# Optimization experiments

Measured on AMD Instinct MI355X. Metric: run time of the kernel, lower is better.

## Reference

```python
import jax, jax.numpy as jnp
import numpy as np
from functools import partial

WIDTH = 2560
LRU = 2560
HEADS = 8
DCONV = 4
B = 4
L = 2048


def setup_inputs() -> dict:
    key = jax.random.key(0)
    ks = jax.random.split(key, 16)
    bw = LRU // HEADS
    x = jax.random.normal(ks[0], (B, L, WIDTH), dtype=jnp.float32)
    segment_pos = jnp.broadcast_to(jnp.arange(L, dtype=jnp.int32), (B, L))
    # indices of the last DCONV frames of the left-padded conv input (length L+DCONV-1)
    base = (jnp.arange(DCONV, dtype=jnp.int32) + (L - 1))
    conv_idx = jnp.broadcast_to(base, (B, LRU, DCONV))
    s = 0.02
    return {
        "x": x,
        "segment_pos": segment_pos,
        "conv_idx": conv_idx,
        "Wx": jax.random.normal(ks[1], (LRU, WIDTH), jnp.float32) * s,
        "bx": jax.random.normal(ks[2], (LRU,), jnp.float32) * s,
        "Wy": jax.random.normal(ks[3], (LRU, WIDTH), jnp.float32) * s,
        "conv_w": jax.random.normal(ks[4], (LRU, DCONV), jnp.float32) * s,  # depthwise kernel
        "conv_b": jax.random.normal(ks[5], (LRU,), jnp.float32) * s,
        "gx_w": jax.random.normal(ks[6], (HEADS, bw, bw), jnp.float32) * s,
        "gx_b": jax.random.normal(ks[7], (HEADS, bw), jnp.float32) * s,
        "ga_w": jax.random.normal(ks[8], (HEADS, bw, bw), jnp.float32) * s,
        "ga_b": jax.random.normal(ks[9], (HEADS, bw), jnp.float32) * s,
        "a_param": jax.random.normal(ks[10], (LRU,), jnp.float32),
        "y_bias": jax.random.normal(ks[11], (1, 1, LRU), jnp.float32) * s,
        "Wout": jax.random.normal(ks[12], (WIDTH, LRU), jnp.float32) * s,
        "bout": jax.random.normal(ks[13], (WIDTH,), jnp.float32) * s,
    }


def _block_diag(x, w):
    # x: [B,L,(h*i)], w: [h,i,j] -> [B,L,(h*j)]
    b, l, _ = x.shape
    h, bw, _ = w.shape
    xb = x.reshape(b, l, h, bw)
    y = jnp.einsum('blhi,hij->blhj', xb, w)
    return y.reshape(b, l, h * bw)


def _scan_op(c1, c2):
    a1, b1 = c1
    a2, b2 = c2
    return (a1 * a2, a2 * b1 + b2)


def reference(x, segment_pos, conv_idx, Wx, bx, Wy, conv_w, conv_b,
              gx_w, gx_b, ga_w, ga_b, a_param, y_bias, Wout, bout):
    dc = conv_w.shape[1]
    seqlen = x.shape[1]

    y = jnp.einsum('bld,ed->ble', x, Wy)                 # linear_y (no bias)
    xl = jnp.einsum('bld,ed->ble', x, Wx) + bx           # linear_x

    # causal depthwise conv1d, padding dc-1 on the left, keep first seqlen
    xpad = jnp.pad(xl, ((0, 0), (dc - 1, 0), (0, 0)))    # [B, L+dc-1, LRU]
    xc = conv_b + sum(conv_w[:, k] * xpad[:, k:k + seqlen, :] for k in range(dc))

    # conv_state: gather of padded (channels-first) input at conv_idx
    conv_state = jnp.take_along_axis(xpad.transpose(0, 2, 1), conv_idx.astype(jnp.int32), axis=2)

    gx = _block_diag(xc, gx_w)  # fuse_bias=True: bias added inside rg_lru
    ga = _block_diag(xc, ga_w)

    # rg_lru_ref
    reset = (segment_pos == 0).astype(x.dtype)[..., None]        # [B,L,1]
    gate_x = jax.nn.sigmoid(gx + gx_b.reshape(-1))
    gate_a = jax.nn.sigmoid(ga + ga_b.reshape(-1))
    c = -8.0 * jax.nn.softplus(a_param)
    log_a = c * gate_a
    a = jnp.exp(log_a) * (1.0 - reset)
    multiplier = jnp.sqrt(1.0 - jnp.exp(2.0 * log_a))
    multiplier = reset + (1.0 - reset) * multiplier
    normalized_x = xc * gate_x * multiplier

    _, h = jax.lax.associative_scan(_scan_op, (a, normalized_x), axis=1)
    last_h = h[:, -1]

    out = h * jax.nn.gelu(y + y_bias, approximate=False)
    out = jnp.einsum('ble,de->bld', out, Wout) + bout    # linear_out
    return out, conv_state, last_h
```

## Files before the change

kernel.cpp:

```cpp
#include <hip/hip_runtime.h>
#include <hip/hip_bf16.h>

#define WIDTH_ 2560
#define LRU_   2560
#define HEADS_ 8
#define BW_    320
#define DCONV_ 4
#define BB     4
#define LL     2048
#define MROWS  (BB*LL)
#define NCH    32
#define CLEN   (LL/NCH)

typedef unsigned short ushort_t;
typedef __attribute__((ext_vector_type(8))) short short8;
typedef __attribute__((ext_vector_type(4))) float f32x4;

__device__ __forceinline__ unsigned short f2bf(float f) {
  union { float f; unsigned u; } v; v.f = f;
  unsigned r = v.u + 0x7fffu + ((v.u >> 16) & 1u);
  return (unsigned short)(r >> 16);
}
__device__ __forceinline__ float bf2f(unsigned short h) {
  union { unsigned u; float f; } v; v.u = ((unsigned)h) << 16;
  return v.f;
}
__device__ __forceinline__ void async_load16(const void* g, void* l) {
  __builtin_amdgcn_global_load_lds(
      (const __attribute__((address_space(1))) unsigned*)g,
      (__attribute__((address_space(3))) unsigned*)l, 16, 0, 0);
}
__device__ __forceinline__ float sigmoidf_(float x) {
  return 1.f / (1.f + __expf(-x));
}

__global__ void cvt_bf16x4(const float4* __restrict__ in, ushort4* __restrict__ out, int n4) {
  int i = blockIdx.x * blockDim.x + threadIdx.x;
  if (i >= n4) return;
  float4 v = in[i];
  ushort4 o;
  o.x = f2bf(v.x); o.y = f2bf(v.y); o.z = f2bf(v.z); o.w = f2bf(v.w);
  out[i] = o;
}

__global__ void cvt_transpose(const float* __restrict__ w, ushort_t* __restrict__ gwT,
                              int rowoff, int n) {
  int i = blockIdx.x * blockDim.x + threadIdx.x;
  if (i >= n) return;
  int ii = i % BW_;
  int j  = (i / BW_) % BW_;
  int h  = i / (BW_ * BW_);
  gwT[((size_t)h * 640 + rowoff + j) * BW_ + ii] = f2bf(w[((size_t)h * BW_ + ii) * BW_ + j]);
}

__global__ void ctab_kernel(const float* __restrict__ apar, float* __restrict__ ctab) {
  int e = blockIdx.x * blockDim.x + threadIdx.x;
  if (e >= LRU_) return;
  float ap = apar[e];
  float sp = (ap > 15.f) ? ap : log1pf(expf(ap));
  ctab[e] = -8.f * sp;
}

template<int EPI>
__global__ __launch_bounds__(512, 2)
void gemm8p(const ushort_t* __restrict__ A,
            const ushort_t* __restrict__ B,
            void* __restrict__ C0, void* __restrict__ C1,
            const float* __restrict__ bias) {
  constexpr int LDA = 2560, KK = 2560, NT = KK / 64, MT = 32;
  __shared__ char smem[131072];
  const int tid = threadIdx.x;
  const int lane = tid & 63, w = tid >> 6;
  const int wr = w >> 2, wc = w & 3;
  const int l15 = lane & 15, l4 = lane >> 4;

  const int nblk = gridDim.x;
  const int bid = blockIdx.x;
  const int swz = (bid & 7) * (nblk >> 3) + (bid >> 3);
  const int tm = (swz % MT) * 256;
  const int tn = (swz / MT) * 256;

  unsigned aoff[4], boff[4]; int ldst[4];
#pragma unroll
  for (int h = 0; h < 2; ++h)
#pragma unroll
    for (int j = 0; j < 2; ++j) {
      int lb = (j * 512 + tid) * 16;
      int lbl = lb ^ (((lb >> 9) & 1) << 5);
      int row = lbl >> 7, colb = lbl & 127;
      aoff[h * 2 + j] = (unsigned)(tm + h * 128 + row) * (LDA * 2) + colb;
      boff[h * 2 + j] = (unsigned)(tn + h * 128 + row) * (KK * 2) + colb;
      ldst[h * 2 + j] = h * 16384 + lb;
    }

  auto STAGE_A = [&](int kt, int p) {
#pragma unroll
    for (int u = 0; u < 4; ++u)
      async_load16((const char*)A + (size_t)aoff[u] + (unsigned)kt * 128,
                   smem + p * 32768 + ldst[u]);
  };
  auto STAGE_B = [&](int kt, int p) {
#pragma unroll
    for (int u = 0; u < 4; ++u)
      async_load16((const char*)B + (size_t)boff[u] + (unsigned)kt * 128,
                   smem + 65536 + p * 32768 + ldst[u]);
  };
  auto LDFRAG = [&](const char* half, int row, int sbyte) -> short8 {
    int lb = row * 128 + sbyte;
    lb ^= ((lb >> 9) & 1) << 5;
    return *(const short8*)(half + lb);
  };

  f32x4 acc[8][4] = {};

  STAGE_A(0, 0); STAGE_B(0, 0);
  asm volatile("s_waitcnt vmcnt(0)" ::: "memory");
  __builtin_amdgcn_s_barrier();

  for (int t = 0; t < NT; ++t) {
    const int p = t & 1;
    const char* Ah = smem + p * 32768 + wr * 16384;
    const char* Bh = smem + 65536 + p * 32768 + (wc >> 1) * 16384;
    const int bcol0 = (wc & 1) * 64;
    short8 bfrag[4][2];
    const bool st = (t + 1 < NT);
#pragma unroll
    for (int q = 0; q < 4; ++q) {
      short8 a[2][2];
#pragma unroll
      for (int mm = 0; mm < 2; ++mm)
#pragma unroll
        for (int s = 0; s < 2; ++s)
          a[mm][s] = LDFRAG(Ah, (2 * q + mm) * 16 + l15, s * 64 + l4 * 16);
      if (q == 0) {
#pragma unroll
        for (int n = 0; n < 4; ++n)
#pragma unroll
          for (int s = 0; s < 2; ++s)
            bfrag[n][s] = LDFRAG(Bh, bcol0 + n * 16 + l15, s * 64 + l4 * 16);
        if (st) STAGE_A(t + 1, p ^ 1);
      }
      if (q == 1 && st) STAGE_B(t + 1, p ^ 1);
      __builtin_amdgcn_s_barrier();
      __builtin_amdgcn_s_setprio(1);
#pragma unroll
      for (int mm = 0; mm < 2; ++mm)
#pragma unroll
        for (int n = 0; n < 4; ++n)
#pragma unroll
          for (int s = 0; s < 2; ++s)
            acc[2 * q + mm][n] = __builtin_amdgcn_mfma_f32_16x16x32_bf16(
                a[mm][s], bfrag[n][s], acc[2 * q + mm][n], 0, 0, 0);
      __builtin_amdgcn_s_setprio(0);
      if (q == 3) asm volatile("s_waitcnt vmcnt(0)" ::: "memory");
      __builtin_amdgcn_s_barrier();
    }
  }

  const int crow0 = tm + wr * 128 + l4 * 4;
  const int ccol0 = tn + wc * 64 + l15;
#pragma unroll
  for (int m = 0; m < 8; ++m)
#pragma unroll
    for (int n = 0; n < 4; ++n) {
      const int col = ccol0 + n * 16;
#pragma unroll
      for (int r = 0; r < 4; ++r) {
        const int row = crow0 + m * 16 + r;
        float v = acc[m][n][r];
        if (EPI == 0) {
          ((float*)C0)[(size_t)row * 2560 + col] = v + bias[col];
        } else {
          if (col < 2560)
            ((ushort_t*)C0)[(size_t)row * 2560 + col] = f2bf(v + bias[col]);
          else
            ((ushort_t*)C1)[(size_t)row * 2560 + (col - 2560)] = f2bf(v);
        }
      }
    }
}

__global__ __launch_bounds__(256, 2)
void gate_gemm(const ushort_t* __restrict__ A,
               const ushort_t* __restrict__ Bw,
               ushort_t* __restrict__ GX,
               ushort_t* __restrict__ AAo,
               const float* __restrict__ gxb, const float* __restrict__ gab,
               const float* __restrict__ ctab, const int* __restrict__ seg) {
  constexpr int BM = 128, BN = 64, BK = 32, WTN = 32, NF = 2;
  __shared__ ushort_t lds_a[BM * BK];
  __shared__ ushort_t lds_b[BN * BK];

  const int tid = threadIdx.x;
  const int w = tid >> 6, lane = tid & 63;
  const int wr = w >> 1, wc = w & 1;
  const int tm = blockIdx.x * BM;
  const int tn = blockIdx.y * BN;
  const int z = blockIdx.z;
  const ushort_t* Ab = A + (size_t)z * BW_;
  const ushort_t* Bb = Bw + (size_t)z * 640 * BW_ + (size_t)tn * BW_;

  f32x4 acc[4][NF] = {};
  const int ksub = (lane >> 4) * 8;
  const int rA = wr * 64 + (lane & 15);
  const int rB = wc * WTN + (lane & 15);

  for (int k0 = 0; k0 < BW_; k0 += BK) {
#pragma unroll
    for (int i = 0; i < 2; ++i) {
      int bo = (i * 256 + tid) * 16;
      int row = bo >> 6, colb = bo & 63;
      async_load16((const char*)Ab + (size_t)(tm + row) * LRU_ * 2 + (size_t)k0 * 2 + colb,
                   (char*)lds_a + bo);
    }
    {
      int bo = tid * 16;
      int row = bo >> 6, colb = bo & 63;
      async_load16((const char*)Bb + (size_t)row * BW_ * 2 + (size_t)k0 * 2 + colb,
                   (char*)lds_b + bo);
    }
    __syncthreads();
    short8 af[4], bfr[NF];
#pragma unroll
    for (int mf = 0; mf < 4; ++mf)
      af[mf] = *(const short8*)&lds_a[(rA + mf * 16) * BK + ksub];
#pragma unroll
    for (int nf = 0; nf < NF; ++nf)
      bfr[nf] = *(const short8*)&lds_b[(rB + nf * 16) * BK + ksub];
#pragma unroll
    for (int mf = 0; mf < 4; ++mf)
#pragma unroll
      for (int nf = 0; nf < NF; ++nf)
        acc[mf][nf] = __builtin_amdgcn_mfma_f32_16x16x32_bf16(af[mf], bfr[nf], acc[mf][nf], 0, 0, 0);
    __syncthreads();
  }

  const int crow0 = tm + wr * 64 + ((lane >> 4) << 2);
  const int ccol0 = tn + wc * WTN + (lane & 15);
#pragma unroll
  for (int mf = 0; mf < 4; ++mf) {
#pragma unroll
    for (int nf = 0; nf < NF; ++nf) {
      const int cih = ccol0 + nf * 16;
#pragma unroll
      for (int r = 0; r < 4; ++r) {
        const int row = crow0 + mf * 16 + r;
        if (cih < BW_) {
          const int gc = z * BW_ + cih;
          float v = acc[mf][nf][r] + gxb[gc];
          float xc = bf2f(A[(size_t)row * LRU_ + gc]);
          GX[(size_t)row * LRU_ + gc] = f2bf(xc * sigmoidf_(v));
        } else {
          const int gc = z * BW_ + cih - BW_;
          float v = acc[mf][nf][r] + gab[gc];
          float la = ctab[gc] * sigmoidf_(v);
          float av = (seg[row] == 0) ? 0.f : expf(la);
          AAo[(size_t)row * LRU_ + gc] = f2bf(av);
        }
      }
    }
  }
}

__global__ void conv_kernel(const ushort_t* __restrict__ xl, const float* __restrict__ convw,
                            const float* __restrict__ convb, ushort_t* __restrict__ xcbf) {
  int i = blockIdx.x * blockDim.x + threadIdx.x;
  if (i >= MROWS * LRU_ / 8) return;
  int e0 = (i % (LRU_ / 8)) * 8;
  int t = (i / (LRU_ / 8)) % LL;
  int b = i / ((LRU_ / 8) * LL);
  size_t rowb = ((size_t)b * LL + t) * LRU_;
  const ushort_t* base = xl + rowb + e0;
  short8 v0 = {}, v1 = {}, v2 = {}, v3;
  if (t >= 3) v0 = *(const short8*)(base - 3 * LRU_);
  if (t >= 2) v1 = *(const short8*)(base - 2 * LRU_);
  if (t >= 1) v2 = *(const short8*)(base - 1 * LRU_);
  v3 = *(const short8*)(base);
  ushort_t o[8];
#pragma unroll
  for (int u = 0; u < 8; ++u) {
    float4 wv = ((const float4*)convw)[e0 + u];
    float acc = convb[e0 + u];
    acc += wv.x * bf2f((ushort_t)v0[u]);
    acc += wv.y * bf2f((ushort_t)v1[u]);
    acc += wv.z * bf2f((ushort_t)v2[u]);
    acc += wv.w * bf2f((ushort_t)v3[u]);
    o[u] = f2bf(acc);
  }
  *(short8*)(xcbf + rowb + e0) = *(short8*)o;
}

__global__ void conv_state_kernel(const ushort_t* __restrict__ xl, const int* __restrict__ cidx,
                                  float* __restrict__ cs) {
  int i = blockIdx.x * blockDim.x + threadIdx.x;
  if (i >= BB * LRU_ * DCONV_) return;
  int e = (i / DCONV_) % LRU_;
  int b = i / (DCONV_ * LRU_);
  int idx = cidx[i];
  int ts = idx - (DCONV_ - 1);
  float v = 0.f;
  if (ts >= 0 && ts < LL) v = bf2f(xl[((size_t)b * LL + ts) * LRU_ + e]);
  cs[i] = v;
}

__global__ void scanA(const ushort_t* __restrict__ AA, const ushort_t* __restrict__ GX,
                      float* __restrict__ cA, float* __restrict__ cH) {
  int i = blockIdx.x * blockDim.x + threadIdx.x;
  if (i >= BB * NCH * LRU_) return;
  int e = i % LRU_;
  int c = (i / LRU_) % NCH;
  int b = i / (LRU_ * NCH);
  float Ap = 1.f, h = 0.f;
  size_t base = ((size_t)b * LL + (size_t)c * CLEN) * LRU_ + e;
  for (int t = 0; t < CLEN; ++t) {
    size_t j = base + (size_t)t * LRU_;
    float a = bf2f(AA[j]);
    float nx = bf2f(GX[j]) * sqrtf(fmaxf(0.f, 1.f - a * a));
    Ap *= a;
    h = a * h + nx;
  }
  cA[i] = Ap; cH[i] = h;
}

__global__ void scanB(const float* __restrict__ cA, const float* __restrict__ cH,
                      float* __restrict__ hInit) {
  int i = blockIdx.x * blockDim.x + threadIdx.x;
  if (i >= BB * LRU_) return;
  int e = i % LRU_;
  int b = i / LRU_;
  float h = 0.f;
  for (int c = 0; c < NCH; ++c) {
    size_t j = ((size_t)b * NCH + c) * LRU_ + e;
    hInit[j] = h;
    h = cA[j] * h + cH[j];
  }
}

__global__ void scanC(const ushort_t* __restrict__ AA, const ushort_t* __restrict__ GXpre,
                      const float* __restrict__ hInit, const ushort_t* __restrict__ ybf,
                      const float* __restrict__ ybias, float* __restrict__ lastH) {
  int i = blockIdx.x * blockDim.x + threadIdx.x;
  if (i >= BB * NCH * LRU_) return;
  int e = i % LRU_;
  int c = (i / LRU_) % NCH;
  int b = i / (LRU_ * NCH);
  float h = hInit[i];
  float yb = ybias[e];
  ushort_t* pre = (ushort_t*)GXpre;
  size_t base = ((size_t)b * LL + (size_t)c * CLEN) * LRU_ + e;
  for (int t = 0; t < CLEN; ++t) {
    size_t j = base + (size_t)t * LRU_;
    float a = bf2f(AA[j]);
    float nx = bf2f(GXpre[j]) * sqrtf(fmaxf(0.f, 1.f - a * a));
    h = a * h + nx;
    float yv = bf2f(ybf[j]) + yb;
    float g = 0.5f * yv * (1.f + erff(yv * 0.70710678118f));
    pre[j] = f2bf(h * g);
  }
  if (c == NCH - 1) lastH[(size_t)b * LRU_ + e] = h;
}

extern "C" void kernel_launch(void* const* d_in, const int* in_sizes, int n_in,
                              void* d_out, int out_size, void* d_ws, size_t ws_size,
                              hipStream_t stream) {
  const float* x     = (const float*)d_in[0];
  const int*   seg   = (const int*)d_in[1];
  const int*   cidx  = (const int*)d_in[2];
  const float* Wx    = (const float*)d_in[3];
  const float* bx    = (const float*)d_in[4];
  const float* Wy    = (const float*)d_in[5];
  const float* convw = (const float*)d_in[6];
  const float* convb = (const float*)d_in[7];
  const float* gxw   = (const float*)d_in[8];
  const float* gxb   = (const float*)d_in[9];
  const float* gaw   = (const float*)d_in[10];
  const float* gab   = (const float*)d_in[11];
  const float* apar  = (const float*)d_in[12];
  const float* ybias = (const float*)d_in[13];
  const float* Wout  = (const float*)d_in[14];
  const float* bout  = (const float*)d_in[15];

  float* out    = (float*)d_out;
  float* cs_out = out + (size_t)MROWS * WIDTH_;
  float* lh_out = cs_out + (size_t)BB * LRU_ * DCONV_;

  ushort_t* ybf = (ushort_t*)d_out;
  ushort_t* AA  = (ushort_t*)((char*)d_out + (size_t)41943040);

  const size_t SZ_BIG = (size_t)MROWS * LRU_ * 2;
  const size_t SZ_WC  = (size_t)(2 * LRU_) * WIDTH_ * 2;
  const size_t SZ_GW  = (size_t)HEADS_ * 640 * BW_ * 2;
  const size_t SZ_SM  = (size_t)BB * NCH * LRU_ * 4;
  size_t need = SZ_BIG * 3 + SZ_WC + SZ_GW + 10240 + SZ_SM * 3;
  if (ws_size < need) return;

  char* p = (char*)d_ws;
  ushort_t* xbf   = (ushort_t*)p; p += SZ_BIG;
  ushort_t* wcat  = (ushort_t*)p; p += SZ_WC;
  ushort_t* T2    = (ushort_t*)p; p += SZ_BIG;
  ushort_t* xcbf  = (ushort_t*)p; p += SZ_BIG;
  ushort_t* gwT   = (ushort_t*)p; p += SZ_GW;
  float*    ctab  = (float*)p;    p += 10240;
  float*    cA    = (float*)p;    p += SZ_SM;
  float*    cH    = (float*)p;    p += SZ_SM;
  float*    hInit = (float*)p;    p += SZ_SM;
  ushort_t* woutbf = wcat;

  const int BLK = 256;
  cvt_bf16x4<<<(MROWS * WIDTH_ / 4 + BLK - 1) / BLK, BLK, 0, stream>>>(
      (const float4*)x, (ushort4*)xbf, MROWS * WIDTH_ / 4);
  cvt_bf16x4<<<(LRU_ * WIDTH_ / 4 + BLK - 1) / BLK, BLK, 0, stream>>>(
      (const float4*)Wx, (ushort4*)wcat, LRU_ * WIDTH_ / 4);
  cvt_bf16x4<<<(LRU_ * WIDTH_ / 4 + BLK - 1) / BLK, BLK, 0, stream>>>(
      (const float4*)Wy, (ushort4*)(wcat + (size_t)LRU_ * WIDTH_), LRU_ * WIDTH_ / 4);

  gemm8p<1><<<640, 512, 0, stream>>>(xbf, wcat, T2, ybf, bx);

  cvt_bf16x4<<<(WIDTH_ * LRU_ / 4 + BLK - 1) / BLK, BLK, 0, stream>>>(
      (const float4*)Wout, (ushort4*)woutbf, WIDTH_ * LRU_ / 4);

  conv_kernel<<<(MROWS * LRU_ / 8 + BLK - 1) / BLK, BLK, 0, stream>>>(T2, convw, convb, xcbf);
  conv_state_kernel<<<(BB * LRU_ * DCONV_ + BLK - 1) / BLK, BLK, 0, stream>>>(T2, cidx, cs_out);

  cvt_transpose<<<(HEADS_ * BW_ * BW_ + BLK - 1) / BLK, BLK, 0, stream>>>(gxw, gwT, 0, HEADS_ * BW_ * BW_);
  cvt_transpose<<<(HEADS_ * BW_ * BW_ + BLK - 1) / BLK, BLK, 0, stream>>>(gaw, gwT, BW_, HEADS_ * BW_ * BW_);
  ctab_kernel<<<(LRU_ + BLK - 1) / BLK, BLK, 0, stream>>>(apar, ctab);

  gate_gemm<<<dim3(MROWS / 128, 10, HEADS_), BLK, 0, stream>>>(
      xcbf, gwT, T2, AA, gxb, gab, ctab, seg);

  scanA<<<(BB * NCH * LRU_ + BLK - 1) / BLK, BLK, 0, stream>>>(AA, T2, cA, cH);
  scanB<<<(BB * LRU_ + BLK - 1) / BLK, BLK, 0, stream>>>(cA, cH, hInit);
  scanC<<<(BB * NCH * LRU_ + BLK - 1) / BLK, BLK, 0, stream>>>(AA, T2, hInit, ybf, ybias, lh_out);

  gemm8p<0><<<320, 512, 0, stream>>>(T2, woutbf, out, nullptr, bout);
}
```

Before: 685.9 us.

## Rework bf16 GEMM main loop into 4-stage BK=32 async-copy ring

The GEMM main loop changes from a double-buffered 64-wide K step with 8 barriers per step to a 4-slot ring of 32-wide K slices. Loads run three stages ahead with graded vmcnt waits and a single barrier per step. The shared-memory layout becomes k-chunk-major with no XOR swizzle, so fragment reads are simple strided 16-byte loads. The block-to-tile mapping is also rewritten. The goal is to cut barrier and synchronisation overhead and hide global-load latency better. The cost is smaller K steps and more outstanding memory operations per wavefront.

```diff
diff --git a/kernel.cpp b/kernel.cpp
--- a/kernel.cpp
+++ b/kernel.cpp
@@ -67,7 +67,7 @@
             const ushort_t* __restrict__ B,
             void* __restrict__ C0, void* __restrict__ C1,
             const float* __restrict__ bias) {
-  constexpr int LDA = 2560, KK = 2560, NT = KK / 64, MT = 32;
+  constexpr int KK = 2560, NT = KK / 32;
   __shared__ char smem[131072];
   const int tid = threadIdx.x;
   const int lane = tid & 63, w = tid >> 6;
@@ -75,86 +75,74 @@
   const int l15 = lane & 15, l4 = lane >> 4;
 
   const int nblk = gridDim.x;
-  const int bid = blockIdx.x;
-  const int swz = (bid & 7) * (nblk >> 3) + (bid >> 3);
-  const int tm = (swz % MT) * 256;
-  const int tn = (swz / MT) * 256;
-
-  unsigned aoff[4], boff[4]; int ldst[4];
-#pragma unroll
-  for (int h = 0; h < 2; ++h)
-#pragma unroll
-    for (int j = 0; j < 2; ++j) {
-      int lb = (j * 512 + tid) * 16;
-      int lbl = lb ^ (((lb >> 9) & 1) << 5);
-      int row = lbl >> 7, colb = lbl & 127;
-      aoff[h * 2 + j] = (unsigned)(tm + h * 128 + row) * (LDA * 2) + colb;
-      boff[h * 2 + j] = (unsigned)(tn + h * 128 + row) * (KK * 2) + colb;
-      ldst[h * 2 + j] = h * 16384 + lb;
-    }
-
-  auto STAGE_A = [&](int kt, int p) {
-#pragma unroll
-    for (int u = 0; u < 4; ++u)
-      async_load16((const char*)A + (size_t)aoff[u] + (unsigned)kt * 128,
-                   smem + p * 32768 + ldst[u]);
-  };
-  auto STAGE_B = [&](int kt, int p) {
-#pragma unroll
-    for (int u = 0; u < 4; ++u)
-      async_load16((const char*)B + (size_t)boff[u] + (unsigned)kt * 128,
-                   smem + 65536 + p * 32768 + ldst[u]);
-  };
-  auto LDFRAG = [&](const char* half, int row, int sbyte) -> short8 {
-    int lb = row * 128 + sbyte;
-    lb ^= ((lb >> 9) & 1) << 5;
-    return *(const short8*)(half + lb);
-  };
+  const int TN = nblk >> 5;
+  const int x8 = blockIdx.x & 7, c = blockIdx.x >> 3;
+  const int tm = (x8 * 4 + c / TN) * 256;
+  const int tn = (c % TN) * 256;
+
+  const char* aSrc[2]; const char* bSrc[2]; int ldst[2];
+#pragma unroll
+  for (int u = 0; u < 2; ++u) {
+    int lb = (u * 512 + tid) * 16;
+    int ks = lb >> 12, m = (lb >> 4) & 255;
+    aSrc[u] = (const char*)A + (size_t)(tm + m) * (KK * 2) + ks * 16;
+    bSrc[u] = (const char*)B + (size_t)(tn + m) * (KK * 2) + ks * 16;
+    ldst[u] = lb;
+  }
 
   f32x4 acc[8][4] = {};
 
-  STAGE_A(0, 0); STAGE_B(0, 0);
-  asm volatile("s_waitcnt vmcnt(0)" ::: "memory");
-  __builtin_amdgcn_s_barrier();
+#pragma unroll
+  for (int kt = 0; kt < 3; ++kt)
+#pragma unroll
+    for (int u = 0; u < 2; ++u) {
+      async_load16(aSrc[u] + kt * 64, smem + kt * 16384 + ldst[u]);
+      async_load16(bSrc[u] + kt * 64, smem + 65536 + kt * 16384 + ldst[u]);
+    }
+
+  const int aRd = (l4 * 256 + wr * 128 + l15) * 16;
+  const int bRd = (l4 * 256 + wc * 64 + l15) * 16 + 65536;
 
   for (int t = 0; t < NT; ++t) {
-    const int p = t & 1;
-    const char* Ah = smem + p * 32768 + wr * 16384;
-    const char* Bh = smem + 65536 + p * 32768 + (wc >> 1) * 16384;
-    const int bcol0 = (wc & 1) * 64;
-    short8 bfrag[4][2];
-    const bool st = (t + 1 < NT);
-#pragma unroll
-    for (int q = 0; q < 4; ++q) {
-      short8 a[2][2];
-#pragma unroll
-      for (int mm = 0; mm < 2; ++mm)
-#pragma unroll
-        for (int s = 0; s < 2; ++s)
-          a[mm][s] = LDFRAG(Ah, (2 * q + mm) * 16 + l15, s * 64 + l4 * 16);
-      if (q == 0) {
-#pragma unroll
-        for (int n = 0; n < 4; ++n)
-#pragma unroll
-          for (int s = 0; s < 2; ++s)
-            bfrag[n][s] = LDFRAG(Bh, bcol0 + n * 16 + l15, s * 64 + l4 * 16);
-        if (st) STAGE_A(t + 1, p ^ 1);
+    if (t < NT - 2)       asm volatile("s_waitcnt vmcnt(8)" ::: "memory");
+    else if (t == NT - 2) asm volatile("s_waitcnt vmcnt(4)" ::: "memory");
+    else                  asm volatile("s_waitcnt vmcnt(0)" ::: "memory");
+    __builtin_amdgcn_s_barrier();
+    if (t + 3 < NT) {
+      const int kt = t + 3, p = kt & 3;
+#pragma unroll
+      for (int u = 0; u < 2; ++u) {
+        async_load16(aSrc[u] + kt * 64, smem + p * 16384 + ldst[u]);
+        async_load16(bSrc[u] + kt * 64, smem + 65536 + p * 16384 + ldst[u]);
       }
-      if (q == 1 && st) STAGE_B(t + 1, p ^ 1);
-      __builtin_amdgcn_s_barrier();
-      __builtin_amdgcn_s_setprio(1);
-#pragma unroll
-      for (int mm = 0; mm < 2; ++mm)
-#pragma unroll
-        for (int n = 0; n < 4; ++n)
-#pragma unroll
-          for (int s = 0; s < 2; ++s)
-            acc[2 * q + mm][n] = __builtin_amdgcn_mfma_f32_16x16x32_bf16(
-                a[mm][s], bfrag[n][s], acc[2 * q + mm][n], 0, 0, 0);
-      __builtin_amdgcn_s_setprio(0);
-      if (q == 3) asm volatile("s_waitcnt vmcnt(0)" ::: "memory");
-      __builtin_amdgcn_s_barrier();
-    }
+    }
+    const char* base = smem + (t & 3) * 16384;
+    short8 bfrag[4], afrag[4];
+#pragma unroll
+    for (int nf = 0; nf < 4; ++nf)
+      bfrag[nf] = *(const short8*)(base + bRd + nf * 256);
+#pragma unroll
+    for (int mf = 0; mf < 4; ++mf)
+      afrag[mf] = *(const short8*)(base + aRd + mf * 256);
+    __builtin_amdgcn_s_setprio(1);
+#pragma unroll
+    for (int mf = 0; mf < 4; ++mf)
+#pragma unroll
+      for (int nf = 0; nf < 4; ++nf)
+        acc[mf][nf] = __builtin_amdgcn_mfma_f32_16x16x32_bf16(
+            afrag[mf], bfrag[nf], acc[mf][nf], 0, 0, 0);
+    __builtin_amdgcn_s_setprio(0);
+#pragma unroll
+    for (int mf = 0; mf < 4; ++mf)
+      afrag[mf] = *(const short8*)(base + aRd + 1024 + mf * 256);
+    __builtin_amdgcn_s_setprio(1);
+#pragma unroll
+    for (int mf = 0; mf < 4; ++mf)
+#pragma unroll
+      for (int nf = 0; nf < 4; ++nf)
+        acc[4 + mf][nf] = __builtin_amdgcn_mfma_f32_16x16x32_bf16(
+            afrag[mf], bfrag[nf], acc[4 + mf][nf], 0, 0, 0);
+    __builtin_amdgcn_s_setprio(0);
   }
 
   const int crow0 = tm + wr * 128 + l4 * 4;
```

Measured after the change: 980.6 us. +43.0%, slower.
